# Kernel optimization log

Measured on AMD Instinct MI355X. Metric: run time of the kernel, lower is better.

The kernel has to match this reference:

```python
import jax, jax.numpy as jnp
from jax import lax
import numpy as np

BN_EPS = 1e-3  # Keras BatchNormalization default epsilon

@jax.custom_vjp
def ste_sign(x):
    # larq ste_sign: sign with sign(0)=+1
    return jnp.where(x >= 0, 1.0, -1.0).astype(x.dtype)

def _ste_fwd(x):
    return ste_sign(x), x

def _ste_bwd(x, g):
    # straight-through estimator: pass grad where |x| <= 1
    return (g * (jnp.abs(x) <= 1.0).astype(g.dtype),)

ste_sign.defvjp(_ste_fwd, _ste_bwd)

def setup_inputs() -> dict:
    key = jax.random.key(0)
    ks = jax.random.split(key, 6)
    x = jax.random.normal(ks[0], (64, 2048, 128), dtype=jnp.float32)
    kernel = jax.random.normal(ks[1], (3, 128, 256), dtype=jnp.float32) * 0.05
    bias = jax.random.normal(ks[2], (256,), dtype=jnp.float32) * 0.01
    beta = jax.random.normal(ks[3], (256,), dtype=jnp.float32) * 0.01
    moving_mean = jax.random.normal(ks[4], (256,), dtype=jnp.float32) * 0.1
    moving_var = jax.random.uniform(ks[5], (256,), dtype=jnp.float32) + 0.5  # positive
    return {"x": x, "kernel": kernel, "bias": bias, "beta": beta,
            "moving_mean": moving_mean, "moving_var": moving_var}

def reference(x, kernel, bias, beta, moving_mean, moving_var):
    # QuantConv1D: binarize input and kernel, then valid conv, stride 1
    xq = ste_sign(x)                 # [B, T, Cin]
    kq = ste_sign(kernel)            # [K, Cin, Cout]
    y = lax.conv_general_dilated(
        xq, kq, window_strides=(1,), padding='VALID',
        dimension_numbers=('NWC', 'WIO', 'NWC'))  # [B, T-K+1, Cout]
    y = y + bias
    # BatchNormalization, inference mode (training=False), scale=False -> no gamma
    inv = lax.rsqrt(moving_var + BN_EPS)
    return (y - moving_mean) * inv + beta
```

## Files before the change

### kernel.cpp

```cpp
#include <hip/hip_runtime.h>
#include <stdint.h>


#define B 64
#define T 2048
#define CIN 128
#define COUT 256
#define KW 3
#define TOUT (T - KW + 1)
#define TW 16
#define NWIN 128
#define WPB 4

typedef float f32x4 __attribute__((ext_vector_type(4)));

__global__ __launch_bounds__(256) void pack_w_kernel(const float* __restrict__ ker,
                                                     const float* __restrict__ bias,
                                                     const float* __restrict__ beta,
                                                     const float* __restrict__ mean,
                                                     const float* __restrict__ var,
                                                     uint32_t* __restrict__ kbT,
                                                     float* __restrict__ A,
                                                     float* __restrict__ C) {
    int k  = blockIdx.x >> 2;
    int i  = blockIdx.x & 3;
    int co = threadIdx.x;
    const float* src = ker + ((size_t)(k * CIN + i)) * COUT + co;
    uint32_t wbits = 0;
    #pragma unroll 8
    for (int bb = 0; bb < 32; ++bb) {
        if (src[(size_t)(4 * bb) * COUT] >= 0.0f) wbits |= (1u << bb);
    }
    kbT[(size_t)co * 12 + k * 4 + i] = wbits;
    if (blockIdx.x == 0) {
        float inv = 1.0f / sqrtf(var[co] + 1e-3f);
        A[co] = -2.0f * inv;
        C[co] = (384.0f + bias[co] - mean[co]) * inv + beta[co];
    }
}

__device__ __forceinline__ int popc4(uint32_t a0, uint32_t a1, uint32_t a2,
                                     uint32_t a3, uint4 k) {
    return __popc(a0 ^ k.x) + __popc(a1 ^ k.y) + __popc(a2 ^ k.z) + __popc(a3 ^ k.w);
}

__global__ __launch_bounds__(256, 6) void conv_kernel(const float* __restrict__ x,
                                                      const uint32_t* __restrict__ kbT,
                                                      const float* __restrict__ A,
                                                      const float* __restrict__ C,
                                                      float* __restrict__ out) {
    const int l   = threadIdx.x & 63;
    const int wv  = threadIdx.x >> 6;
    const int gw  = blockIdx.x * WPB + wv;
    const int b   = gw >> 7;
    const int win = gw & (NWIN - 1);
    const int t0  = (win < NWIN - 1) ? win * TW : (TOUT - TW);

    const int co0 = l * 4;
    uint4 kj[4][KW];
    #pragma unroll
    for (int j = 0; j < 4; ++j)
        #pragma unroll
        for (int k = 0; k < KW; ++k)
            kj[j][k] = *(const uint4*)(kbT + (size_t)(co0 + j) * 12 + k * 4);
    const float4 av = *(const float4*)(A + co0);
    const float4 cv = *(const float4*)(C + co0);

    const float* xb0 = x + (size_t)b * T * CIN;
    const int l4 = l * 4;
    auto loadpair = [&](int r) -> float4 {
        r = (r > T - 2) ? (T - 2) : r;
        return *(const float4*)(xb0 + (size_t)r * CIN + l4);
    };

    float4 v0 = loadpair(t0);
    float4 v  = loadpair(t0 + 2);
    uint64_t p0 = __ballot(v0.x >= 0.0f);
    uint64_t p1 = __ballot(v0.y >= 0.0f);
    uint64_t p2 = __ballot(v0.z >= 0.0f);
    uint64_t p3 = __ballot(v0.w >= 0.0f);

    float* orow = out + ((size_t)b * TOUT + t0) * COUT + co0;

    #pragma unroll 2
    for (int j = 0; j < TW / 2; ++j) {
        float4 vn = loadpair(t0 + 2 * j + 4);

        uint64_t m0 = __ballot(v.x >= 0.0f);
        uint64_t m1 = __ballot(v.y >= 0.0f);
        uint64_t m2 = __ballot(v.z >= 0.0f);
        uint64_t m3 = __ballot(v.w >= 0.0f);

        uint32_t r0a = (uint32_t)p0,         r0b = (uint32_t)p1,         r0c = (uint32_t)p2,         r0d = (uint32_t)p3;
        uint32_t r1a = (uint32_t)(p0 >> 32), r1b = (uint32_t)(p1 >> 32), r1c = (uint32_t)(p2 >> 32), r1d = (uint32_t)(p3 >> 32);
        uint32_t r2a = (uint32_t)m0,         r2b = (uint32_t)m1,         r2c = (uint32_t)m2,         r2d = (uint32_t)m3;
        uint32_t r3a = (uint32_t)(m0 >> 32), r3b = (uint32_t)(m1 >> 32), r3c = (uint32_t)(m2 >> 32), r3d = (uint32_t)(m3 >> 32);

        f32x4 o0, o1;
        #pragma unroll
        for (int jj = 0; jj < 4; ++jj) {
            int s0 = popc4(r0a, r0b, r0c, r0d, kj[jj][0])
                   + popc4(r1a, r1b, r1c, r1d, kj[jj][1])
                   + popc4(r2a, r2b, r2c, r2d, kj[jj][2]);
            int s1 = popc4(r1a, r1b, r1c, r1d, kj[jj][0])
                   + popc4(r2a, r2b, r2c, r2d, kj[jj][1])
                   + popc4(r3a, r3b, r3c, r3d, kj[jj][2]);
            float aj = (&av.x)[jj], cj = (&cv.x)[jj];
            o0[jj] = fmaf((float)s0, aj, cj);
            o1[jj] = fmaf((float)s1, aj, cj);
        }

        float* op = orow + (size_t)(2 * j) * COUT;
        __builtin_nontemporal_store(o0, (f32x4*)op);
        __builtin_nontemporal_store(o1, (f32x4*)(op + COUT));

        p0 = m0; p1 = m1; p2 = m2; p3 = m3;
        v = vn;
    }
}

extern "C" void kernel_launch(void* const* d_in, const int* in_sizes, int n_in,
                              void* d_out, int out_size, void* d_ws, size_t ws_size,
                              hipStream_t stream) {
    const float* x    = (const float*)d_in[0];
    const float* ker  = (const float*)d_in[1];
    const float* bias = (const float*)d_in[2];
    const float* beta = (const float*)d_in[3];
    const float* mean = (const float*)d_in[4];
    const float* var  = (const float*)d_in[5];
    float* out = (float*)d_out;

    uint32_t* kbT = (uint32_t*)d_ws;
    float*    A   = (float*)(kbT + (size_t)COUT * 12);
    float*    C   = A + COUT;

    pack_w_kernel<<<KW * 4, 256, 0, stream>>>(ker, bias, beta, mean, var, kbT, A, C);
    conv_kernel<<<(B * NWIN) / WPB, 256, 0, stream>>>(x, kbT, A, C, out);
}
```

Measured before the change: 44.01 us.

## Prepack binarized input rows in a separate kernel and widen conv time windows

```diff
diff --git a/kernel.cpp b/kernel.cpp
--- a/kernel.cpp
+++ b/kernel.cpp
@@ -8,9 +8,10 @@
 #define COUT 256
 #define KW 3
 #define TOUT (T - KW + 1)
-#define TW 16
-#define NWIN 128
+#define TW 32
+#define NWIN 64
 #define WPB 4
+#define PACK_ROWS 32
 
 typedef float f32x4 __attribute__((ext_vector_type(4)));
 
@@ -39,20 +40,44 @@
     }
 }
 
-__device__ __forceinline__ int popc4(uint32_t a0, uint32_t a1, uint32_t a2,
-                                     uint32_t a3, uint4 k) {
-    return __popc(a0 ^ k.x) + __popc(a1 ^ k.y) + __popc(a2 ^ k.z) + __popc(a3 ^ k.w);
+__global__ __launch_bounds__(256) void pack_x_kernel(const float* __restrict__ x,
+                                                     uint4* __restrict__ xb) {
+    const int l   = threadIdx.x & 63;
+    const int wid = blockIdx.x * WPB + (threadIdx.x >> 6);
+    const size_t row0 = (size_t)wid * PACK_ROWS;
+    const float* p = x + row0 * CIN + l * 4;
+    uint4* q = xb + row0;
+
+    #pragma unroll 4
+    for (int i = 0; i < PACK_ROWS / 2; ++i) {
+        float4 v = *(const float4*)(p + (size_t)i * 2 * CIN);
+        uint64_t m0 = __ballot(v.x >= 0.0f);
+        uint64_t m1 = __ballot(v.y >= 0.0f);
+        uint64_t m2 = __ballot(v.z >= 0.0f);
+        uint64_t m3 = __ballot(v.w >= 0.0f);
+        if (l == 0) {
+            q[2 * i] = make_uint4((uint32_t)m0, (uint32_t)m1,
+                                  (uint32_t)m2, (uint32_t)m3);
+        } else if (l == 1) {
+            q[2 * i + 1] = make_uint4((uint32_t)(m0 >> 32), (uint32_t)(m1 >> 32),
+                                      (uint32_t)(m2 >> 32), (uint32_t)(m3 >> 32));
+        }
+    }
 }
 
-__global__ __launch_bounds__(256, 6) void conv_kernel(const float* __restrict__ x,
-                                                      const uint32_t* __restrict__ kbT,
-                                                      const float* __restrict__ A,
-                                                      const float* __restrict__ C,
-                                                      float* __restrict__ out) {
+__device__ __forceinline__ int popc4(uint4 r, uint4 k) {
+    return __popc(r.x ^ k.x) + __popc(r.y ^ k.y) + __popc(r.z ^ k.z) + __popc(r.w ^ k.w);
+}
+
+__global__ __launch_bounds__(256) void conv_kernel(const uint4* __restrict__ xb,
+                                                   const uint32_t* __restrict__ kbT,
+                                                   const float* __restrict__ A,
+                                                   const float* __restrict__ C,
+                                                   float* __restrict__ out) {
     const int l   = threadIdx.x & 63;
     const int wv  = threadIdx.x >> 6;
     const int gw  = blockIdx.x * WPB + wv;
-    const int b   = gw >> 7;
+    const int b   = gw >> 6;
     const int win = gw & (NWIN - 1);
     const int t0  = (win < NWIN - 1) ? win * TW : (TOUT - TW);
 
@@ -66,56 +91,40 @@
     const float4 av = *(const float4*)(A + co0);
     const float4 cv = *(const float4*)(C + co0);
 
-    const float* xb0 = x + (size_t)b * T * CIN;
-    const int l4 = l * 4;
-    auto loadpair = [&](int r) -> float4 {
-        r = (r > T - 2) ? (T - 2) : r;
-        return *(const float4*)(xb0 + (size_t)r * CIN + l4);
-    };
-
-    float4 v0 = loadpair(t0);
-    float4 v  = loadpair(t0 + 2);
-    uint64_t p0 = __ballot(v0.x >= 0.0f);
-    uint64_t p1 = __ballot(v0.y >= 0.0f);
-    uint64_t p2 = __ballot(v0.z >= 0.0f);
-    uint64_t p3 = __ballot(v0.w >= 0.0f);
-
+    const uint4* xr = xb + (size_t)b * T + t0;
     float* orow = out + ((size_t)b * TOUT + t0) * COUT + co0;
 
+    uint4 r0 = xr[0];
+    uint4 r1 = xr[1];
     #pragma unroll 2
-    for (int j = 0; j < TW / 2; ++j) {
-        float4 vn = loadpair(t0 + 2 * j + 4);
+    for (int j = 0; j < TW / 4; ++j) {
+        uint4 r2 = xr[4 * j + 2];
+        uint4 r3 = xr[4 * j + 3];
+        uint4 r4 = xr[4 * j + 4];
+        uint4 r5 = xr[4 * j + 5];
 
-        uint64_t m0 = __ballot(v.x >= 0.0f);
-        uint64_t m1 = __ballot(v.y >= 0.0f);
-        uint64_t m2 = __ballot(v.z >= 0.0f);
-        uint64_t m3 = __ballot(v.w >= 0.0f);
-
-        uint32_t r0a = (uint32_t)p0,         r0b = (uint32_t)p1,         r0c = (uint32_t)p2,         r0d = (uint32_t)p3;
-        uint32_t r1a = (uint32_t)(p0 >> 32), r1b = (uint32_t)(p1 >> 32), r1c = (uint32_t)(p2 >> 32), r1d = (uint32_t)(p3 >> 32);
-        uint32_t r2a = (uint32_t)m0,         r2b = (uint32_t)m1,         r2c = (uint32_t)m2,         r2d = (uint32_t)m3;
-        uint32_t r3a = (uint32_t)(m0 >> 32), r3b = (uint32_t)(m1 >> 32), r3c = (uint32_t)(m2 >> 32), r3d = (uint32_t)(m3 >> 32);
-
-        f32x4 o0, o1;
+        f32x4 o0, o1, o2, o3;
         #pragma unroll
         for (int jj = 0; jj < 4; ++jj) {
-            int s0 = popc4(r0a, r0b, r0c, r0d, kj[jj][0])
-                   + popc4(r1a, r1b, r1c, r1d, kj[jj][1])
-                   + popc4(r2a, r2b, r2c, r2d, kj[jj][2]);
-            int s1 = popc4(r1a, r1b, r1c, r1d, kj[jj][0])
-                   + popc4(r2a, r2b, r2c, r2d, kj[jj][1])
-                   + popc4(r3a, r3b, r3c, r3d, kj[jj][2]);
+            int s0 = popc4(r0, kj[jj][0]) + popc4(r1, kj[jj][1]) + popc4(r2, kj[jj][2]);
+            int s1 = popc4(r1, kj[jj][0]) + popc4(r2, kj[jj][1]) + popc4(r3, kj[jj][2]);
+            int s2 = popc4(r2, kj[jj][0]) + popc4(r3, kj[jj][1]) + popc4(r4, kj[jj][2]);
+            int s3 = popc4(r3, kj[jj][0]) + popc4(r4, kj[jj][1]) + popc4(r5, kj[jj][2]);
             float aj = (&av.x)[jj], cj = (&cv.x)[jj];
             o0[jj] = fmaf((float)s0, aj, cj);
             o1[jj] = fmaf((float)s1, aj, cj);
+            o2[jj] = fmaf((float)s2, aj, cj);
+            o3[jj] = fmaf((float)s3, aj, cj);
         }
 
-        float* op = orow + (size_t)(2 * j) * COUT;
+        float* op = orow + (size_t)(4 * j) * COUT;
         __builtin_nontemporal_store(o0, (f32x4*)op);
         __builtin_nontemporal_store(o1, (f32x4*)(op + COUT));
+        __builtin_nontemporal_store(o2, (f32x4*)(op + 2 * COUT));
+        __builtin_nontemporal_store(o3, (f32x4*)(op + 3 * COUT));
 
-        p0 = m0; p1 = m1; p2 = m2; p3 = m3;
-        v = vn;
+        r0 = r4;
+        r1 = r5;
     }
 }
 
@@ -133,7 +142,9 @@
     uint32_t* kbT = (uint32_t*)d_ws;
     float*    A   = (float*)(kbT + (size_t)COUT * 12);
     float*    C   = A + COUT;
+    uint4*    xb  = (uint4*)(C + COUT);
 
+    pack_x_kernel<<<(B * T / PACK_ROWS) / WPB, 256, 0, stream>>>(x, xb);
     pack_w_kernel<<<KW * 4, 256, 0, stream>>>(ker, bias, beta, mean, var, kbT, A, C);
-    conv_kernel<<<(B * NWIN) / WPB, 256, 0, stream>>>(x, kbT, A, C, out);
+    conv_kernel<<<(B * NWIN) / WPB, 256, 0, stream>>>(xb, kbT, A, C, out);
 }
```

Result: slower. 55.07 us (+25.1%).
